# Optimization experiments

Measured on AMD Instinct MI355X. Metric: run time of the kernel, lower is better.

The kernel has to match this reference:

```python
import math
import jax, jax.numpy as jnp
import numpy as np

H, PQ, PV, E, C, S, N = 12, 4, 8, 16, 128, 384, 512


def setup_inputs() -> dict:
    key = jax.random.key(0)
    ks = jax.random.split(key, 16)
    rn = lambda k, shape, scale=1.0: jax.random.normal(k, shape, jnp.float32) * scale
    single = rn(ks[0], (N, S))
    pair = rn(ks[1], (N, N, C))
    R, _ = jnp.linalg.qr(rn(ks[2], (N, 3, 3)))  # proper orthonormal frames
    t = rn(ks[3], (N, 3))
    w = 0.02
    return dict(
        single_representation=single,
        pair_representation=pair,
        rotations=R,
        translations=t,
        Wq=rn(ks[4], (H, S, E), w),
        Wk=rn(ks[5], (H, S, E), w),
        Wv=rn(ks[6], (H, S, E), w),
        Wqp=rn(ks[7], (H, PQ, S, 3), w),
        Wkp=rn(ks[8], (H, PQ, S, 3), w),
        Wvp=rn(ks[9], (H, PV, S, 3), w),
        Wb=rn(ks[10], (H, C), w),
        Wout=rn(ks[11], (H * (C + E + PV * 4), S), w),
        b_out=jnp.zeros((S,), jnp.float32),
        scale_head=jnp.ones((H,), jnp.float32),
    )


def _frame_apply(R, t, pts):
    # R:[N,3,3], t:[N,3], pts:[H,P,N,3] -> R_n @ p + t_n per residue n
    return jnp.einsum('nij,hpnj->hpni', R, pts) + t[None, None, :, :]


def reference(single_representation, pair_representation, rotations, translations,
              Wq, Wk, Wv, Wqp, Wkp, Wvp, Wb, Wout, b_out, scale_head):
    single, pair = single_representation, pair_representation
    n = single.shape[0]

    # --- sequence QK term ---
    q = jnp.einsum('nd,hde->hne', single, Wq)
    k = jnp.einsum('nd,hde->hne', single, Wk)
    w_single = math.sqrt(1.0 / E) * jnp.einsum('hne,hme->hnm', q, k)  # [H,N,N]

    # --- pair bias term ---
    w_pair = jnp.einsum('nmc,hc->hnm', pair, Wb)  # [H,N,N]

    # --- frame (3D point distance) term ---
    qp = jnp.einsum('nd,hpdk->hpnk', single, Wqp)  # [H,PQ,N,3]
    kp = jnp.einsum('nd,hpdk->hpnk', single, Wkp)
    lqp = _frame_apply(rotations, translations, qp)
    lkp = _frame_apply(rotations, translations, kp)
    diff = lqp[:, :, :, None, :] - lkp[:, :, None, :, :]   # [H,PQ,N,N,3]
    sqd = jnp.sum(diff * diff, axis=(1, 4))                 # [H,N,N] (sum over points & xyz)
    w_frame = (-math.sqrt(1.0 / (18 * PQ))) * jax.nn.softplus(scale_head)[:, None, None] * sqd

    w = jax.nn.softmax(w_single + w_pair + w_frame, axis=-1)  # [H,N,N]

    # --- sequence value aggregation ---
    v = jnp.einsum('nd,hde->hne', single, Wv)
    att_single = jnp.einsum('hnm,hme->hne', w, v)             # [H,N,E]
    att_single = jnp.transpose(att_single, (1, 0, 2)).reshape(n, -1)

    # --- pair value aggregation (faithful to source: sums over query index too) ---
    colsum = jnp.sum(w, axis=1)                               # [H,N] = sum_a w[h,a,b]
    att_pair = jnp.einsum('hb,ibc->hic', colsum, pair)        # [H,N,C]
    att_pair = jnp.transpose(att_pair, (1, 0, 2)).reshape(n, -1)

    # --- 3D point value aggregation ---
    vp = jnp.einsum('nd,hpdk->hpnk', single, Wvp)             # [H,PV,N,3]
    lvp = _frame_apply(rotations, translations, vp)
    local_out = jnp.einsum('hnm,hpmk->hpnk', w, lvp)          # [H,PV,N,3]
    Rinv = jnp.swapaxes(rotations, -1, -2)                    # R^T
    tinv = -jnp.einsum('nij,nj->ni', Rinv, translations)      # -R^T t
    global_out = _frame_apply(Rinv, tinv, local_out)          # [H,PV,N,3]
    out_points = jnp.transpose(global_out, (2, 1, 0, 3)).reshape(n, -1)  # [N, PV*H*3]
    out_norm = jnp.linalg.norm(global_out, axis=-1)           # [H,PV,N]
    out_norm = jnp.transpose(out_norm, (2, 1, 0)).reshape(n, -1)         # [N, PV*H]

    att = jnp.concatenate([att_single, att_pair, out_points, out_norm], axis=-1)
    return att @ Wout + b_out
```

## Files before the change

kernel.cpp:

```cpp
#include <hip/hip_runtime.h>
#include <math.h>

#define NRES 512
#define HH 12
#define PQn 4
#define PVn 8
#define En 16
#define Cn 128
#define Sn 384
#define ATT_COLS 2112

#define OFF_Q    0
#define OFF_K    (OFF_Q   + HH*NRES*En)
#define OFF_V    (OFF_K   + HH*NRES*En)
#define OFF_LQP  (OFF_V   + HH*NRES*En)
#define OFF_LKP  (OFF_LQP + HH*NRES*12)
#define OFF_LVP  (OFF_LKP + HH*NRES*12)
#define OFF_CS   (OFF_LVP + HH*NRES*24)
#define OFF_ATT  (OFF_CS  + NRES*HH)
#define OFF_LG   (OFF_ATT + NRES*ATT_COLS)
#define OFF_PART OFF_LG
#define OFF_KC   OFF_ATT
#define OFF_D1   (OFF_KC + NRES*HH*28)
#define OFF_D0   (OFF_D1 + NRES*HH)
#define OFF_QC   (OFF_D0 + NRES*HH)
#define KSPLIT 16
#define KCHUNK (ATT_COLS/KSPLIT)
#define OROWS 8

__global__ __launch_bounds__(256) void ipa_proj(
    const float* __restrict__ single, const float* __restrict__ Rm,
    const float* __restrict__ tr,
    const float* __restrict__ Wq, const float* __restrict__ Wk,
    const float* __restrict__ Wv, const float* __restrict__ Wqp,
    const float* __restrict__ Wkp, const float* __restrict__ Wvp,
    float* __restrict__ ws)
{
  float* q   = ws + OFF_Q;  float* k   = ws + OFF_K;  float* v   = ws + OFF_V;
  float* lqp = ws + OFF_LQP; float* lkp = ws + OFF_LKP; float* lvp = ws + OFF_LVP;
  const int n0 = blockIdx.x * 8;
  const int g  = blockIdx.y;
  const int tid = threadIdx.x;
  __shared__ float sS[8][388];
  __shared__ float sR[8][9];
  __shared__ float sT[8][3];
  #pragma unroll
  for (int i = 0; i < 3; ++i) {
    int idx = i*256 + tid;
    int r = idx / 96, c4 = idx % 96;
    float4 val = *reinterpret_cast<const float4*>(single + (size_t)(n0 + r)*Sn + c4*4);
    *reinterpret_cast<float4*>(&sS[r][c4*4]) = val;
  }
  if (tid < 72)      sR[tid/9][tid%9] = Rm[(size_t)(n0 + tid/9)*9 + tid%9];
  else if (tid < 96) { int r = (tid-72)/3; sT[r][(tid-72)%3] = tr[(size_t)(n0+r)*3 + (tid-72)%3]; }
  __syncthreads();
  #pragma unroll
  for (int i = 0; i < 3; ++i) {
    int item = i*256 + tid;
    int nl = item & 7;
    int ul = item >> 3;
    int u  = g*96 + ul;
    const float* srow = sS[nl];
    if (u < 576) {
      int which = u/192, r = u%192, h = r>>4, e = r&15;
      const float* W = (which==0 ? Wq : which==1 ? Wk : Wv) + (size_t)h*Sn*En + e;
      float acc = 0.f;
      #pragma unroll 8
      for (int d = 0; d < Sn; ++d) acc = fmaf(srow[d], W[(size_t)d*En], acc);
      float* dst = (which==0 ? q : which==1 ? k : v);
      dst[((size_t)h*NRES + (n0+nl))*En + e] = acc;
    } else {
      int u2 = u - 576;
      const float* W; float* dst;
      if (u2 < 48)      { int h=u2>>2,     p=u2&3;      W = Wqp + (size_t)(h*PQn+p)*Sn*3; dst = lqp + ((size_t)h*NRES + (n0+nl))*12 + p*3; }
      else if (u2 < 96) { int h=(u2-48)>>2,p=(u2-48)&3; W = Wkp + (size_t)(h*PQn+p)*Sn*3; dst = lkp + ((size_t)h*NRES + (n0+nl))*12 + p*3; }
      else              { int h=(u2-96)>>3,p=(u2-96)&7; W = Wvp + (size_t)(h*PVn+p)*Sn*3; dst = lvp + ((size_t)h*NRES + (n0+nl))*24 + p*3; }
      float x0=0.f,x1=0.f,x2=0.f;
      #pragma unroll 4
      for (int d = 0; d < Sn; ++d) {
        float sv = srow[d];
        x0 = fmaf(sv, W[d*3+0], x0);
        x1 = fmaf(sv, W[d*3+1], x1);
        x2 = fmaf(sv, W[d*3+2], x2);
      }
      const float* R8 = sR[nl]; const float* T8 = sT[nl];
      dst[0] = R8[0]*x0 + R8[1]*x1 + R8[2]*x2 + T8[0];
      dst[1] = R8[3]*x0 + R8[4]*x1 + R8[5]*x2 + T8[1];
      dst[2] = R8[6]*x0 + R8[7]*x1 + R8[8]*x2 + T8[2];
    }
  }
}

__global__ __launch_bounds__(256) void ipa_pack(
    const float* __restrict__ scale_head, float* __restrict__ ws)
{
  const float* q   = ws + OFF_Q;
  const float* k   = ws + OFF_K;
  const float* lkp = ws + OFF_LKP;
  const float* lqp = ws + OFF_LQP;
  float* kc = ws + OFF_KC;
  float* qc = ws + OFF_QC;
  float* d1 = ws + OFF_D1;
  float* d0 = ws + OFF_D0;
  const int idx = blockIdx.x*256 + threadIdx.x;
  const int h = idx >> 9, m = idx & 511;
  const float gamma = 0.11785113019775793f * log1pf(__expf(scale_head[h]));
  const float* kr  = k   + ((size_t)h*NRES + m)*En;
  const float* qr  = q   + ((size_t)h*NRES + m)*En;
  const float* lkr = lkp + ((size_t)h*NRES + m)*12;
  const float* lqr = lqp + ((size_t)h*NRES + m)*12;
  float* kcr = kc + ((size_t)m*HH + h)*28;
  float* qcr = qc + ((size_t)m*HH + h)*28;
  #pragma unroll
  for (int e = 0; e < En; ++e) { kcr[e] = 0.25f * kr[e]; qcr[e] = qr[e]; }
  float Bm = 0.f, An = 0.f;
  #pragma unroll
  for (int j = 0; j < 12; ++j) {
    float b = lkr[j], a = lqr[j];
    kcr[16+j] = (2.f*gamma)*b;
    qcr[16+j] = a;
    Bm = fmaf(b, b, Bm);
    An = fmaf(a, a, An);
  }
  d1[m*HH + h] = -gamma*Bm;
  d0[m*HH + h] = -gamma*An;
}

__global__ __launch_bounds__(256) void ipa_logits(
    const float* __restrict__ pair, const float* __restrict__ Wb,
    float* __restrict__ ws)
{
  const float* kc = ws + OFF_KC;
  const float* qc = ws + OFF_QC;
  const float* d1 = ws + OFF_D1;
  const float* d0 = ws + OFF_D0;
  float* lg = ws + OFF_LG;

  __shared__ float sWb[HH*Cn];
  __shared__ float sOut[HH*68];
  for (int i = threadIdx.x; i < HH*Cn/4; i += 256)
    reinterpret_cast<float4*>(sWb)[i] = reinterpret_cast<const float4*>(Wb)[i];
  __syncthreads();

  const int n    = blockIdx.x;
  const int tid  = threadIdx.x;
  const int lane = tid & 63;
  const int wave = tid >> 6;
  const int r    = lane >> 2;
  const int cq   = lane & 3;
  const int ml   = wave*16 + r;
  const int m    = blockIdx.y*64 + ml;

  const float* p1 = pair + ((size_t)n*NRES + m)*Cn + cq*4;

  float acc[HH];
  #pragma unroll
  for (int h = 0; h < HH; ++h) acc[h] = 0.f;

  #pragma unroll
  for (int jg = 0; jg < 8; ++jg) {
    float4 pv = *reinterpret_cast<const float4*>(p1 + jg*16);
    #pragma unroll
    for (int h = 0; h < HH; ++h) {
      const float4 wb = *reinterpret_cast<const float4*>(&sWb[h*Cn + jg*16 + cq*4]);
      acc[h] += pv.x*wb.x + pv.y*wb.y + pv.z*wb.z + pv.w*wb.w;
    }
  }
  #pragma unroll
  for (int h = 0; h < HH; ++h) {
    acc[h] += __shfl_xor(acc[h], 1);
    acc[h] += __shfl_xor(acc[h], 2);
  }
  float b0, b1, b2;
  if      (cq == 0) { b0=acc[0]; b1=acc[1];  b2=acc[2];  }
  else if (cq == 1) { b0=acc[3]; b1=acc[4];  b2=acc[5];  }
  else if (cq == 2) { b0=acc[6]; b1=acc[7];  b2=acc[8];  }
  else              { b0=acc[9]; b1=acc[10]; b2=acc[11]; }

  const int hb = 3*cq;
  const float* kc1 = kc + ((size_t)m*HH + hb)*28;
  const float* qcn = qc + ((size_t)n*HH + hb)*28;
  const float* d0n = d0 + (size_t)n*HH + hb;
  const float* d11 = d1 + (size_t)m*HH + hb;

  #pragma unroll
  for (int i = 0; i < 3; ++i) {
    float t = (i==0 ? b0 : i==1 ? b1 : b2) + d11[i] + d0n[i];
    #pragma unroll
    for (int j = 0; j < 7; ++j) {
      float4 qv = *reinterpret_cast<const float4*>(qcn + i*28 + j*4);
      float4 k1 = *reinterpret_cast<const float4*>(kc1 + i*28 + j*4);
      t += k1.x*qv.x + k1.y*qv.y + k1.z*qv.z + k1.w*qv.w;
    }
    sOut[(hb+i)*68 + ml] = t;
  }
  __syncthreads();
  if (tid < HH*16) {
    const int h = tid >> 4, q4 = tid & 15;
    float4 o = make_float4(sOut[h*68 + q4*4 + 0], sOut[h*68 + q4*4 + 1],
                           sOut[h*68 + q4*4 + 2], sOut[h*68 + q4*4 + 3]);
    *reinterpret_cast<float4*>(
        lg + ((size_t)h*NRES + n)*NRES + blockIdx.y*64 + q4*4) = o;
  }
}

__global__ __launch_bounds__(256) void ipa_smagg(
    const float* __restrict__ Rm, const float* __restrict__ tr,
    float* __restrict__ ws)
{
  const float* v   = ws + OFF_V;
  const float* lvp = ws + OFF_LVP;
  float* lg  = ws + OFF_LG;
  float* att = ws + OFF_ATT;
  const int row  = blockIdx.x*4 + (threadIdx.x >> 6);
  const int lane = threadIdx.x & 63;
  const int h = row >> 9, n = row & 511;

  float4* p = reinterpret_cast<float4*>(lg + (size_t)row*NRES);
  float4 x0 = p[lane];
  float4 x1 = p[64 + lane];
  float mx = fmaxf(fmaxf(fmaxf(x0.x,x0.y),fmaxf(x0.z,x0.w)),
                   fmaxf(fmaxf(x1.x,x1.y),fmaxf(x1.z,x1.w)));
  #pragma unroll
  for (int off = 32; off >= 1; off >>= 1) mx = fmaxf(mx, __shfl_xor(mx, off));
  x0.x = __expf(x0.x-mx); x0.y = __expf(x0.y-mx); x0.z = __expf(x0.z-mx); x0.w = __expf(x0.w-mx);
  x1.x = __expf(x1.x-mx); x1.y = __expf(x1.y-mx); x1.z = __expf(x1.z-mx); x1.w = __expf(x1.w-mx);
  float sum = x0.x+x0.y+x0.z+x0.w + x1.x+x1.y+x1.z+x1.w;
  #pragma unroll
  for (int off = 32; off >= 1; off >>= 1) sum += __shfl_xor(sum, off);
  const float inv = 1.f/sum;
  x0.x*=inv; x0.y*=inv; x0.z*=inv; x0.w*=inv;
  x1.x*=inv; x1.y*=inv; x1.z*=inv; x1.w*=inv;
  p[lane] = x0;
  p[64 + lane] = x1;

  float wv[8] = {x0.x, x0.y, x0.z, x0.w, x1.x, x1.y, x1.z, x1.w};
  float acc[40];
  #pragma unroll
  for (int i = 0; i < 40; ++i) acc[i] = 0.f;
  #pragma unroll
  for (int jj = 0; jj < 8; ++jj) {
    const int col = (jj < 4) ? (4*lane + jj) : (256 + 4*lane + (jj-4));
    const float w = wv[jj];
    const float4* v4 = reinterpret_cast<const float4*>(v + ((size_t)h*NRES + col)*En);
    float4 a0=v4[0], a1=v4[1], a2=v4[2], a3=v4[3];
    acc[0]+=w*a0.x; acc[1]+=w*a0.y; acc[2]+=w*a0.z; acc[3]+=w*a0.w;
    acc[4]+=w*a1.x; acc[5]+=w*a1.y; acc[6]+=w*a1.z; acc[7]+=w*a1.w;
    acc[8]+=w*a2.x; acc[9]+=w*a2.y; acc[10]+=w*a2.z; acc[11]+=w*a2.w;
    acc[12]+=w*a3.x; acc[13]+=w*a3.y; acc[14]+=w*a3.z; acc[15]+=w*a3.w;
    const float4* l4 = reinterpret_cast<const float4*>(lvp + ((size_t)h*NRES + col)*24);
    #pragma unroll
    for (int t = 0; t < 6; ++t) {
      float4 b = l4[t];
      acc[16+4*t+0]+=w*b.x; acc[16+4*t+1]+=w*b.y;
      acc[16+4*t+2]+=w*b.z; acc[16+4*t+3]+=w*b.w;
    }
  }
  #pragma unroll
  for (int off = 32; off >= 1; off >>= 1) {
    #pragma unroll
    for (int i = 0; i < 40; ++i) acc[i] += __shfl_xor(acc[i], off);
  }
  if (lane == 0) {
    size_t ab = (size_t)n*ATT_COLS;
    float4* as = reinterpret_cast<float4*>(att + ab + h*En);
    as[0] = make_float4(acc[0],acc[1],acc[2],acc[3]);
    as[1] = make_float4(acc[4],acc[5],acc[6],acc[7]);
    as[2] = make_float4(acc[8],acc[9],acc[10],acc[11]);
    as[3] = make_float4(acc[12],acc[13],acc[14],acc[15]);
    const float R0=Rm[n*9+0],R1=Rm[n*9+1],R2=Rm[n*9+2],
                R3=Rm[n*9+3],R4=Rm[n*9+4],R5=Rm[n*9+5],
                R6=Rm[n*9+6],R7=Rm[n*9+7],R8=Rm[n*9+8];
    const float t0=tr[n*3+0], t1=tr[n*3+1], t2=tr[n*3+2];
    #pragma unroll
    for (int pp = 0; pp < 8; ++pp) {
      float d0 = acc[16+3*pp+0]-t0, d1 = acc[16+3*pp+1]-t1, d2 = acc[16+3*pp+2]-t2;
      float g0 = R0*d0 + R3*d1 + R6*d2;
      float g1 = R1*d0 + R4*d1 + R7*d2;
      float g2 = R2*d0 + R5*d1 + R8*d2;
      att[ab + 1728 + (pp*HH + h)*3 + 0] = g0;
      att[ab + 1728 + (pp*HH + h)*3 + 1] = g1;
      att[ab + 1728 + (pp*HH + h)*3 + 2] = g2;
      att[ab + 2016 + pp*HH + h] = sqrtf(g0*g0 + g1*g1 + g2*g2);
    }
  }
}

__global__ __launch_bounds__(256) void ipa_colsum(float* __restrict__ ws)
{
  const float* lg = ws + OFF_LG;
  float* cs = ws + OFF_CS;
  const int h = blockIdx.x, ac = blockIdx.y, tid = threadIdx.x;
  const float* base = lg + (size_t)h*NRES*NRES + (size_t)ac*64*NRES;
  float acc0 = 0.f, acc1 = 0.f;
  #pragma unroll 4
  for (int a = 0; a < 64; ++a) {
    acc0 += base[(size_t)a*NRES + tid];
    acc1 += base[(size_t)a*NRES + tid + 256];
  }
  atomicAdd(&cs[(size_t)tid*HH + h],       acc0);
  atomicAdd(&cs[(size_t)(tid+256)*HH + h], acc1);
}

__global__ __launch_bounds__(256) void ipa_pairagg(
    const float* __restrict__ pair, float* __restrict__ ws)
{
  const float* cs = ws + OFF_CS;
  float* att = ws + OFF_ATT;
  const int i = blockIdx.x, tid = threadIdx.x;
  __shared__ float sCS[NRES*HH];
  __shared__ float4 sRed[4][HH][32];
  #pragma unroll
  for (int it = 0; it < 6; ++it) {
    int idx = it*256 + tid;
    reinterpret_cast<float4*>(sCS)[idx] = reinterpret_cast<const float4*>(cs)[idx];
  }
  __syncthreads();
  const int c4 = tid & 31, bg = tid >> 5;
  const int b0 = bg * 64;
  float4 acc[HH];
  #pragma unroll
  for (int h = 0; h < HH; ++h) acc[h] = make_float4(0.f,0.f,0.f,0.f);
  const float* prow = pair + (size_t)i*NRES*Cn;
  for (int jb = 0; jb < 64; jb += 4) {
    float4 pv[4];
    #pragma unroll
    for (int u = 0; u < 4; ++u)
      pv[u] = *reinterpret_cast<const float4*>(prow + (size_t)(b0+jb+u)*Cn + c4*4);
    #pragma unroll
    for (int u = 0; u < 4; ++u) {
      const float4* csr = reinterpret_cast<const float4*>(&sCS[(b0+jb+u)*HH]);
      float4 c0 = csr[0], c1 = csr[1], c2 = csr[2];
      float w[12] = {c0.x,c0.y,c0.z,c0.w, c1.x,c1.y,c1.z,c1.w, c2.x,c2.y,c2.z,c2.w};
      #pragma unroll
      for (int h = 0; h < HH; ++h) {
        acc[h].x = fmaf(w[h], pv[u].x, acc[h].x);
        acc[h].y = fmaf(w[h], pv[u].y, acc[h].y);
        acc[h].z = fmaf(w[h], pv[u].z, acc[h].z);
        acc[h].w = fmaf(w[h], pv[u].w, acc[h].w);
      }
    }
  }
  if (bg >= 4) {
    for (int h = 0; h < HH; ++h) sRed[bg-4][h][c4] = acc[h];
  }
  __syncthreads();
  if (bg < 4) {
    for (int h = 0; h < HH; ++h) {
      float4 b2 = sRed[bg][h][c4];
      acc[h].x+=b2.x; acc[h].y+=b2.y; acc[h].z+=b2.z; acc[h].w+=b2.w;
    }
  }
  __syncthreads();
  if (bg >= 2 && bg < 4) {
    for (int h = 0; h < HH; ++h) sRed[bg-2][h][c4] = acc[h];
  }
  __syncthreads();
  if (bg < 2) {
    for (int h = 0; h < HH; ++h) {
      float4 b2 = sRed[bg][h][c4];
      acc[h].x+=b2.x; acc[h].y+=b2.y; acc[h].z+=b2.z; acc[h].w+=b2.w;
    }
  }
  __syncthreads();
  if (bg == 1) {
    for (int h = 0; h < HH; ++h) sRed[0][h][c4] = acc[h];
  }
  __syncthreads();
  if (bg == 0) {
    size_t base = (size_t)i*ATT_COLS + 192;
    for (int h = 0; h < HH; ++h) {
      float4 b2 = sRed[0][h][c4];
      acc[h].x+=b2.x; acc[h].y+=b2.y; acc[h].z+=b2.z; acc[h].w+=b2.w;
      *reinterpret_cast<float4*>(att + base + h*Cn + c4*4) = acc[h];
    }
  }
}

__global__ __launch_bounds__(384) void ipa_outp(
    const float* __restrict__ att, const float* __restrict__ Wout,
    float* __restrict__ ws)
{
  float* partial = ws + OFF_PART;
  const int rb = blockIdx.x;
  const int ks = blockIdx.y;
  const int s  = threadIdx.x;
  const int n0 = rb*OROWS;
  const int j0 = ks*KCHUNK;

  float acc[OROWS];
  #pragma unroll
  for (int r = 0; r < OROWS; ++r) acc[r] = 0.f;

  for (int jg = 0; jg < KCHUNK/4; ++jg) {
    const int j = j0 + jg*4;
    float w0 = Wout[(size_t)(j+0)*Sn + s];
    float w1 = Wout[(size_t)(j+1)*Sn + s];
    float w2 = Wout[(size_t)(j+2)*Sn + s];
    float w3 = Wout[(size_t)(j+3)*Sn + s];
    #pragma unroll
    for (int r = 0; r < OROWS; ++r) {
      float4 av = *reinterpret_cast<const float4*>(att + (size_t)(n0+r)*ATT_COLS + j);
      acc[r] = fmaf(av.x, w0, acc[r]);
      acc[r] = fmaf(av.y, w1, acc[r]);
      acc[r] = fmaf(av.z, w2, acc[r]);
      acc[r] = fmaf(av.w, w3, acc[r]);
    }
  }
  #pragma unroll
  for (int r = 0; r < OROWS; ++r)
    partial[((size_t)ks*NRES + n0 + r)*Sn + s] = acc[r];
}

__global__ __launch_bounds__(384) void ipa_outred(
    const float* __restrict__ b_out, float* __restrict__ ws,
    float* __restrict__ out)
{
  const float* partial = ws + OFF_PART;
  const int n = blockIdx.x, s = threadIdx.x;
  float a = b_out[s];
  #pragma unroll
  for (int ks = 0; ks < KSPLIT; ++ks)
    a += partial[((size_t)ks*NRES + n)*Sn + s];
  out[(size_t)n*Sn + s] = a;
}

extern "C" void kernel_launch(void* const* d_in, const int* in_sizes, int n_in,
                              void* d_out, int out_size, void* d_ws, size_t ws_size,
                              hipStream_t stream) {
  const float* single = (const float*)d_in[0];
  const float* pair   = (const float*)d_in[1];
  const float* Rm     = (const float*)d_in[2];
  const float* tr     = (const float*)d_in[3];
  const float* Wq     = (const float*)d_in[4];
  const float* Wk     = (const float*)d_in[5];
  const float* Wv     = (const float*)d_in[6];
  const float* Wqp    = (const float*)d_in[7];
  const float* Wkp    = (const float*)d_in[8];
  const float* Wvp    = (const float*)d_in[9];
  const float* Wb     = (const float*)d_in[10];
  const float* Wout   = (const float*)d_in[11];
  const float* b_out  = (const float*)d_in[12];
  const float* scale_head = (const float*)d_in[13];
  float* ws  = (float*)d_ws;
  float* out = (float*)d_out;

  hipMemsetAsync(ws + OFF_CS, 0, NRES*HH*sizeof(float), stream);
  ipa_proj   <<<dim3(64, 8),  256, 0, stream>>>(single, Rm, tr, Wq, Wk, Wv, Wqp, Wkp, Wvp, ws);
  ipa_pack   <<<dim3(24),     256, 0, stream>>>(scale_head, ws);
  ipa_logits <<<dim3(NRES, 8), 256, 0, stream>>>(pair, Wb, ws);
  ipa_smagg  <<<dim3(HH*NRES/4), 256, 0, stream>>>(Rm, tr, ws);
  ipa_colsum <<<dim3(HH, 8),  256, 0, stream>>>(ws);
  ipa_pairagg<<<dim3(NRES),   256, 0, stream>>>(pair, ws);
  ipa_outp   <<<dim3(NRES/OROWS, KSPLIT), 384, 0, stream>>>(ws + OFF_ATT, Wout, ws);
  ipa_outred <<<dim3(NRES),   384, 0, stream>>>(b_out, ws, out);
}
```

Measured before the change: 296.3 us.

## Restructure projection to reuse weights across residues and split softmax from aggregation

The projection kernel now gives each thread one output column for four residues, so every weight load is reused four times. The point-frame transform moves out of it into the pack kernel, which rotates query, key and value points in place. The fused softmax+aggregation kernel is split into a softmax kernel and a separate aggregation kernel that re-reads the normalized weights with coalesced per-lane column access. The split adds one more kernel launch and an extra pass over the logits buffer.

```diff
diff --git a/kernel.cpp b/kernel.cpp
--- a/kernel.cpp
+++ b/kernel.cpp
@@ -9,6 +9,7 @@
 #define Cn 128
 #define Sn 384
 #define ATT_COLS 2112
+#define PUNITS 1152
 
 #define OFF_Q    0
 #define OFF_K    (OFF_Q   + HH*NRES*En)
@@ -29,75 +30,71 @@
 #define OROWS 8
 
 __global__ __launch_bounds__(256) void ipa_proj(
-    const float* __restrict__ single, const float* __restrict__ Rm,
-    const float* __restrict__ tr,
+    const float* __restrict__ single,
     const float* __restrict__ Wq, const float* __restrict__ Wk,
     const float* __restrict__ Wv, const float* __restrict__ Wqp,
     const float* __restrict__ Wkp, const float* __restrict__ Wvp,
     float* __restrict__ ws)
 {
-  float* q   = ws + OFF_Q;  float* k   = ws + OFF_K;  float* v   = ws + OFF_V;
-  float* lqp = ws + OFF_LQP; float* lkp = ws + OFF_LKP; float* lvp = ws + OFF_LVP;
-  const int n0 = blockIdx.x * 8;
-  const int g  = blockIdx.y;
-  const int tid = threadIdx.x;
-  __shared__ float sS[8][388];
-  __shared__ float sR[8][9];
-  __shared__ float sT[8][3];
-  #pragma unroll
-  for (int i = 0; i < 3; ++i) {
-    int idx = i*256 + tid;
+  float* q   = ws + OFF_Q;  float* k   = ws + OFF_K;  float* v = ws + OFF_V;
+  float* rqp = ws + OFF_LQP; float* rkp = ws + OFF_LKP; float* rvp = ws + OFF_LVP;
+  const int n0 = blockIdx.x * 4;
+  const int u  = blockIdx.y * 256 + threadIdx.x;
+  __shared__ float sS[4][388];
+  for (int idx = threadIdx.x; idx < 4*96; idx += 256) {
     int r = idx / 96, c4 = idx % 96;
-    float4 val = *reinterpret_cast<const float4*>(single + (size_t)(n0 + r)*Sn + c4*4);
-    *reinterpret_cast<float4*>(&sS[r][c4*4]) = val;
-  }
-  if (tid < 72)      sR[tid/9][tid%9] = Rm[(size_t)(n0 + tid/9)*9 + tid%9];
-  else if (tid < 96) { int r = (tid-72)/3; sT[r][(tid-72)%3] = tr[(size_t)(n0+r)*3 + (tid-72)%3]; }
-  __syncthreads();
-  #pragma unroll
-  for (int i = 0; i < 3; ++i) {
-    int item = i*256 + tid;
-    int nl = item & 7;
-    int ul = item >> 3;
-    int u  = g*96 + ul;
-    const float* srow = sS[nl];
-    if (u < 576) {
-      int which = u/192, r = u%192, h = r>>4, e = r&15;
-      const float* W = (which==0 ? Wq : which==1 ? Wk : Wv) + (size_t)h*Sn*En + e;
-      float acc = 0.f;
-      #pragma unroll 8
-      for (int d = 0; d < Sn; ++d) acc = fmaf(srow[d], W[(size_t)d*En], acc);
-      float* dst = (which==0 ? q : which==1 ? k : v);
-      dst[((size_t)h*NRES + (n0+nl))*En + e] = acc;
+    *reinterpret_cast<float4*>(&sS[r][c4*4]) =
+        *reinterpret_cast<const float4*>(single + (size_t)(n0+r)*Sn + c4*4);
+  }
+  __syncthreads();
+  if (u >= PUNITS) return;
+
+  const float* W; float* dst; int wstride, dstride;
+  if (u < 576) {
+    int which = u/192, r = u%192, h = r>>4, e = r&15;
+    W = (which==0 ? Wq : which==1 ? Wk : Wv) + (size_t)h*Sn*En + e;
+    dst = (which==0 ? q : which==1 ? k : v) + ((size_t)h*NRES + n0)*En + e;
+    wstride = En; dstride = En;
+  } else {
+    int u2 = u - 576;
+    if (u2 < 144) {
+      int h = u2/12, pk = u2%12;
+      W = Wqp + (size_t)(h*PQn + pk/3)*Sn*3 + (pk%3);
+      dst = rqp + ((size_t)h*NRES + n0)*12 + pk; wstride = 3; dstride = 12;
+    } else if (u2 < 288) {
+      int t = u2-144; int h = t/12, pk = t%12;
+      W = Wkp + (size_t)(h*PQn + pk/3)*Sn*3 + (pk%3);
+      dst = rkp + ((size_t)h*NRES + n0)*12 + pk; wstride = 3; dstride = 12;
     } else {
-      int u2 = u - 576;
-      const float* W; float* dst;
-      if (u2 < 48)      { int h=u2>>2,     p=u2&3;      W = Wqp + (size_t)(h*PQn+p)*Sn*3; dst = lqp + ((size_t)h*NRES + (n0+nl))*12 + p*3; }
-      else if (u2 < 96) { int h=(u2-48)>>2,p=(u2-48)&3; W = Wkp + (size_t)(h*PQn+p)*Sn*3; dst = lkp + ((size_t)h*NRES + (n0+nl))*12 + p*3; }
-      else              { int h=(u2-96)>>3,p=(u2-96)&7; W = Wvp + (size_t)(h*PVn+p)*Sn*3; dst = lvp + ((size_t)h*NRES + (n0+nl))*24 + p*3; }
-      float x0=0.f,x1=0.f,x2=0.f;
-      #pragma unroll 4
-      for (int d = 0; d < Sn; ++d) {
-        float sv = srow[d];
-        x0 = fmaf(sv, W[d*3+0], x0);
-        x1 = fmaf(sv, W[d*3+1], x1);
-        x2 = fmaf(sv, W[d*3+2], x2);
-      }
-      const float* R8 = sR[nl]; const float* T8 = sT[nl];
-      dst[0] = R8[0]*x0 + R8[1]*x1 + R8[2]*x2 + T8[0];
-      dst[1] = R8[3]*x0 + R8[4]*x1 + R8[5]*x2 + T8[1];
-      dst[2] = R8[6]*x0 + R8[7]*x1 + R8[8]*x2 + T8[2];
-    }
-  }
+      int t = u2-288; int h = t/24, pk = t%24;
+      W = Wvp + (size_t)(h*PVn + pk/3)*Sn*3 + (pk%3);
+      dst = rvp + ((size_t)h*NRES + n0)*24 + pk; wstride = 3; dstride = 24;
+    }
+  }
+  float a0=0.f, a1=0.f, a2=0.f, a3=0.f;
+  #pragma unroll 8
+  for (int d = 0; d < Sn; ++d) {
+    float w = W[(size_t)d*wstride];
+    a0 = fmaf(sS[0][d], w, a0);
+    a1 = fmaf(sS[1][d], w, a1);
+    a2 = fmaf(sS[2][d], w, a2);
+    a3 = fmaf(sS[3][d], w, a3);
+  }
+  dst[0]         = a0;
+  dst[dstride]   = a1;
+  dst[2*dstride] = a2;
+  dst[3*dstride] = a3;
 }
 
 __global__ __launch_bounds__(256) void ipa_pack(
-    const float* __restrict__ scale_head, float* __restrict__ ws)
-{
-  const float* q   = ws + OFF_Q;
-  const float* k   = ws + OFF_K;
-  const float* lkp = ws + OFF_LKP;
-  const float* lqp = ws + OFF_LQP;
+    const float* __restrict__ scale_head, const float* __restrict__ Rm,
+    const float* __restrict__ tr, float* __restrict__ ws)
+{
+  const float* q  = ws + OFF_Q;
+  const float* k  = ws + OFF_K;
+  float* rqp = ws + OFF_LQP;
+  float* rkp = ws + OFF_LKP;
+  float* rvp = ws + OFF_LVP;
   float* kc = ws + OFF_KC;
   float* qc = ws + OFF_QC;
   float* d1 = ws + OFF_D1;
@@ -105,10 +102,42 @@
   const int idx = blockIdx.x*256 + threadIdx.x;
   const int h = idx >> 9, m = idx & 511;
   const float gamma = 0.11785113019775793f * log1pf(__expf(scale_head[h]));
-  const float* kr  = k   + ((size_t)h*NRES + m)*En;
-  const float* qr  = q   + ((size_t)h*NRES + m)*En;
-  const float* lkr = lkp + ((size_t)h*NRES + m)*12;
-  const float* lqr = lqp + ((size_t)h*NRES + m)*12;
+  const float R0=Rm[m*9+0],R1=Rm[m*9+1],R2=Rm[m*9+2],
+              R3=Rm[m*9+3],R4=Rm[m*9+4],R5=Rm[m*9+5],
+              R6=Rm[m*9+6],R7=Rm[m*9+7],R8=Rm[m*9+8];
+  const float t0=tr[m*3+0], t1=tr[m*3+1], t2=tr[m*3+2];
+
+  float lq[12], lk[12];
+  {
+    const float* rq = rqp + ((size_t)h*NRES + m)*12;
+    const float* rk = rkp + ((size_t)h*NRES + m)*12;
+    #pragma unroll
+    for (int p = 0; p < 4; ++p) {
+      float x0=rq[p*3+0], x1=rq[p*3+1], x2=rq[p*3+2];
+      lq[p*3+0] = R0*x0 + R1*x1 + R2*x2 + t0;
+      lq[p*3+1] = R3*x0 + R4*x1 + R5*x2 + t1;
+      lq[p*3+2] = R6*x0 + R7*x1 + R8*x2 + t2;
+      float y0=rk[p*3+0], y1=rk[p*3+1], y2=rk[p*3+2];
+      lk[p*3+0] = R0*y0 + R1*y1 + R2*y2 + t0;
+      lk[p*3+1] = R3*y0 + R4*y1 + R5*y2 + t1;
+      lk[p*3+2] = R6*y0 + R7*y1 + R8*y2 + t2;
+    }
+  }
+  {
+    float* rv = rvp + ((size_t)h*NRES + m)*24;
+    float tmp[24];
+    #pragma unroll
+    for (int j = 0; j < 24; ++j) tmp[j] = rv[j];
+    #pragma unroll
+    for (int p = 0; p < 8; ++p) {
+      float x0=tmp[p*3+0], x1=tmp[p*3+1], x2=tmp[p*3+2];
+      rv[p*3+0] = R0*x0 + R1*x1 + R2*x2 + t0;
+      rv[p*3+1] = R3*x0 + R4*x1 + R5*x2 + t1;
+      rv[p*3+2] = R6*x0 + R7*x1 + R8*x2 + t2;
+    }
+  }
+  const float* kr = k + ((size_t)h*NRES + m)*En;
+  const float* qr = q + ((size_t)h*NRES + m)*En;
   float* kcr = kc + ((size_t)m*HH + h)*28;
   float* qcr = qc + ((size_t)m*HH + h)*28;
   #pragma unroll
@@ -116,7 +145,7 @@
   float Bm = 0.f, An = 0.f;
   #pragma unroll
   for (int j = 0; j < 12; ++j) {
-    float b = lkr[j], a = lqr[j];
+    float b = lk[j], a = lq[j];
     kcr[16+j] = (2.f*gamma)*b;
     qcr[16+j] = a;
     Bm = fmaf(b, b, Bm);
@@ -204,18 +233,11 @@
   }
 }
 
-__global__ __launch_bounds__(256) void ipa_smagg(
-    const float* __restrict__ Rm, const float* __restrict__ tr,
-    float* __restrict__ ws)
-{
-  const float* v   = ws + OFF_V;
-  const float* lvp = ws + OFF_LVP;
-  float* lg  = ws + OFF_LG;
-  float* att = ws + OFF_ATT;
+__global__ __launch_bounds__(256) void ipa_softmax(float* __restrict__ ws)
+{
+  float* lg = ws + OFF_LG;
   const int row  = blockIdx.x*4 + (threadIdx.x >> 6);
   const int lane = threadIdx.x & 63;
-  const int h = row >> 9, n = row & 511;
-
   float4* p = reinterpret_cast<float4*>(lg + (size_t)row*NRES);
   float4 x0 = p[lane];
   float4 x1 = p[64 + lane];
@@ -233,27 +255,57 @@
   x1.x*=inv; x1.y*=inv; x1.z*=inv; x1.w*=inv;
   p[lane] = x0;
   p[64 + lane] = x1;
-
-  float wv[8] = {x0.x, x0.y, x0.z, x0.w, x1.x, x1.y, x1.z, x1.w};
+}
+
+__global__ __launch_bounds__(256) void ipa_colsum(float* __restrict__ ws)
+{
+  const float* lg = ws + OFF_LG;
+  float* cs = ws + OFF_CS;
+  const int h = blockIdx.x, ac = blockIdx.y, tid = threadIdx.x;
+  const float* base = lg + (size_t)h*NRES*NRES + (size_t)ac*64*NRES;
+  float acc0 = 0.f, acc1 = 0.f;
+  #pragma unroll 4
+  for (int a = 0; a < 64; ++a) {
+    acc0 += base[(size_t)a*NRES + tid];
+    acc1 += base[(size_t)a*NRES + tid + 256];
+  }
+  atomicAdd(&cs[(size_t)tid*HH + h],       acc0);
+  atomicAdd(&cs[(size_t)(tid+256)*HH + h], acc1);
+}
+
+__global__ __launch_bounds__(256) void ipa_agg(
+    const float* __restrict__ Rm, const float* __restrict__ tr,
+    float* __restrict__ ws)
+{
+  const float* v   = ws + OFF_V;
+  const float* lvp = ws + OFF_LVP;
+  const float* lg  = ws + OFF_LG;
+  float* att = ws + OFF_ATT;
+  const int row  = blockIdx.x*4 + (threadIdx.x >> 6);
+  const int lane = threadIdx.x & 63;
+  const int h = row >> 9, n = row & 511;
+
   float acc[40];
   #pragma unroll
   for (int i = 0; i < 40; ++i) acc[i] = 0.f;
-  #pragma unroll
-  for (int jj = 0; jj < 8; ++jj) {
-    const int col = (jj < 4) ? (4*lane + jj) : (256 + 4*lane + (jj-4));
-    const float w = wv[jj];
-    const float4* v4 = reinterpret_cast<const float4*>(v + ((size_t)h*NRES + col)*En);
+
+  const float* wrow = lg + (size_t)row*NRES;
+  #pragma unroll 2
+  for (int j = 0; j < 8; ++j) {
+    const int m = j*64 + lane;
+    const float wv = wrow[m];
+    const float4* v4 = reinterpret_cast<const float4*>(v + ((size_t)h*NRES + m)*En);
     float4 a0=v4[0], a1=v4[1], a2=v4[2], a3=v4[3];
-    acc[0]+=w*a0.x; acc[1]+=w*a0.y; acc[2]+=w*a0.z; acc[3]+=w*a0.w;
-    acc[4]+=w*a1.x; acc[5]+=w*a1.y; acc[6]+=w*a1.z; acc[7]+=w*a1.w;
-    acc[8]+=w*a2.x; acc[9]+=w*a2.y; acc[10]+=w*a2.z; acc[11]+=w*a2.w;
-    acc[12]+=w*a3.x; acc[13]+=w*a3.y; acc[14]+=w*a3.z; acc[15]+=w*a3.w;
-    const float4* l4 = reinterpret_cast<const float4*>(lvp + ((size_t)h*NRES + col)*24);
+    acc[0]+=wv*a0.x; acc[1]+=wv*a0.y; acc[2]+=wv*a0.z; acc[3]+=wv*a0.w;
+    acc[4]+=wv*a1.x; acc[5]+=wv*a1.y; acc[6]+=wv*a1.z; acc[7]+=wv*a1.w;
+    acc[8]+=wv*a2.x; acc[9]+=wv*a2.y; acc[10]+=wv*a2.z; acc[11]+=wv*a2.w;
+    acc[12]+=wv*a3.x; acc[13]+=wv*a3.y; acc[14]+=wv*a3.z; acc[15]+=wv*a3.w;
+    const float4* l4 = reinterpret_cast<const float4*>(lvp + ((size_t)h*NRES + m)*24);
     #pragma unroll
     for (int t = 0; t < 6; ++t) {
       float4 b = l4[t];
-      acc[16+4*t+0]+=w*b.x; acc[16+4*t+1]+=w*b.y;
-      acc[16+4*t+2]+=w*b.z; acc[16+4*t+3]+=w*b.w;
+      acc[16+4*t+0]+=wv*b.x; acc[16+4*t+1]+=wv*b.y;
+      acc[16+4*t+2]+=wv*b.z; acc[16+4*t+3]+=wv*b.w;
     }
   }
   #pragma unroll
@@ -284,22 +336,6 @@
       att[ab + 2016 + pp*HH + h] = sqrtf(g0*g0 + g1*g1 + g2*g2);
     }
   }
-}
-
-__global__ __launch_bounds__(256) void ipa_colsum(float* __restrict__ ws)
-{
-  const float* lg = ws + OFF_LG;
-  float* cs = ws + OFF_CS;
-  const int h = blockIdx.x, ac = blockIdx.y, tid = threadIdx.x;
-  const float* base = lg + (size_t)h*NRES*NRES + (size_t)ac*64*NRES;
-  float acc0 = 0.f, acc1 = 0.f;
-  #pragma unroll 4
-  for (int a = 0; a < 64; ++a) {
-    acc0 += base[(size_t)a*NRES + tid];
-    acc1 += base[(size_t)a*NRES + tid + 256];
-  }
-  atomicAdd(&cs[(size_t)tid*HH + h],       acc0);
-  atomicAdd(&cs[(size_t)(tid+256)*HH + h], acc1);
 }
 
 __global__ __launch_bounds__(256) void ipa_pairagg(
@@ -446,11 +482,12 @@
   float* out = (float*)d_out;
 
   hipMemsetAsync(ws + OFF_CS, 0, NRES*HH*sizeof(float), stream);
-  ipa_proj   <<<dim3(64, 8),  256, 0, stream>>>(single, Rm, tr, Wq, Wk, Wv, Wqp, Wkp, Wvp, ws);
-  ipa_pack   <<<dim3(24),     256, 0, stream>>>(scale_head, ws);
+  ipa_proj   <<<dim3(128, 5), 256, 0, stream>>>(single, Wq, Wk, Wv, Wqp, Wkp, Wvp, ws);
+  ipa_pack   <<<dim3(24),     256, 0, stream>>>(scale_head, Rm, tr, ws);
   ipa_logits <<<dim3(NRES, 8), 256, 0, stream>>>(pair, Wb, ws);
-  ipa_smagg  <<<dim3(HH*NRES/4), 256, 0, stream>>>(Rm, tr, ws);
+  ipa_softmax<<<dim3(HH*NRES/4), 256, 0, stream>>>(ws);
   ipa_colsum <<<dim3(HH, 8),  256, 0, stream>>>(ws);
+  ipa_agg    <<<dim3(HH*NRES/4), 256, 0, stream>>>(Rm, tr, ws);
   ipa_pairagg<<<dim3(NRES),   256, 0, stream>>>(pair, ws);
   ipa_outp   <<<dim3(NRES/OROWS, KSPLIT), 384, 0, stream>>>(ws + OFF_ATT, Wout, ws);
   ipa_outred <<<dim3(NRES),   384, 0, stream>>>(b_out, ws, out);
```

After: 283.9 us. 4.2% less time.
